# Performance work log

Hardware: AMD Instinct MI355X
Metric: run time of the kernel (lower is better)

The kernel has to match this reference:

```python
import jax, jax.numpy as jnp
import numpy as np

B, S, D, F, E = 4, 2048, 1024, 4096, 4


def setup_inputs() -> dict:
    key = jax.random.key(0)
    ks = jax.random.split(key, 8)
    sd = 1.0 / np.sqrt(D)  # torch Linear default init bound (fan_in = d_model)
    sf = 1.0 / np.sqrt(F)  # fan_in = d_ff
    return {
        "x": jax.random.normal(ks[0], (B, S, D), dtype=jnp.float32),
        # per-expert MLP params, stacked over expert dim E
        "W1": jax.random.uniform(ks[1], (E, D, F), jnp.float32, -sd, sd),
        "b1": jax.random.uniform(ks[2], (E, F), jnp.float32, -sd, sd),
        "W2": jax.random.uniform(ks[3], (E, F, D), jnp.float32, -sf, sf),
        "b2": jax.random.uniform(ks[4], (E, D), jnp.float32, -sf, sf),
        # uncertainty head: Linear(d_model, 1)
        "Wu": jax.random.uniform(ks[5], (D, 1), jnp.float32, -sd, sd),
        "bu": jax.random.uniform(ks[6], (1,), jnp.float32, -sd, sd),
    }


def reference(x, W1, b1, W2, b2, Wu, bu):
    # x: [B, S, D]
    n_exp = W1.shape[0]
    seq = x.shape[1]

    # uncertainty in (0,1), per token: sigmoid(Linear(x)).squeeze(-1)
    u = jax.nn.sigmoid(jnp.einsum("bsd,do->bso", x, Wu) + bu)[..., 0]  # [B,S]
    # variable number of experts per token in [1, E]
    k = jnp.clip(jnp.ceil(u * n_exp), 1, n_exp).astype(jnp.int32)  # [B,S]

    # dense all-expert MLP: every expert processes every token (faithful math;
    # original gathers only active tokens, but per-token result is identical)
    h = jax.nn.relu(jnp.einsum("bsd,edf->bsef", x, W1) + b1)  # [B,S,E,F]
    y = jnp.einsum("bsef,efd->bsed", h, W2) + b2               # [B,S,E,D]

    s_idx = jnp.arange(seq)
    out = jnp.zeros_like(x)
    for i in range(1, n_exp + 1):  # loop over small fixed expert count
        # expert assigned at pass i depends only on position: (s + i - 1) % E
        e_idx = (s_idx + i - 1) % n_exp  # [S]
        y_i = jnp.take_along_axis(y, e_idx[None, :, None, None], axis=2)[:, :, 0, :]  # [B,S,D]
        w = jnp.where(k >= i, u / i, 0.0)  # [B,S]
        out = out + w[..., None] * y_i
    return out
```

## Files before the change

### kernel.cpp

```cpp
#include <hip/hip_runtime.h>

#define DEV __device__ __forceinline__

typedef __attribute__((ext_vector_type(8))) short s16x8;
typedef __attribute__((ext_vector_type(4))) float f32x4;
typedef __attribute__((ext_vector_type(4))) unsigned short u16x4;

#define BTOK 8192
#define DD   1024
#define FF   4096
#define EE   4
#define BK   64

DEV unsigned short f2bf(float f) {
  unsigned int u = __float_as_uint(f);
  unsigned int r = (u + 0x7FFFu + ((u >> 16) & 1u)) >> 16;
  return (unsigned short)r;
}

DEV void gld_lds16(const void* g, void* l) {
  __builtin_amdgcn_global_load_lds(
      (const __attribute__((address_space(1))) unsigned int*)g,
      (__attribute__((address_space(3))) unsigned int*)l,
      16, 0, 0);
}

DEV void gemm_ring(const unsigned short* __restrict__ A,
                   const unsigned short* __restrict__ B,
                   int K, int tileM, int tileN,
                   unsigned short* Ls,
                   f32x4 (&acc)[8][4]) {
  const int t    = threadIdx.x;
  const int lane = t & 63;
  const int wid  = t >> 6;
  const int wr   = wid >> 2;
  const int wc   = wid & 3;
  const int m16  = lane & 15;
  const int quad = lane >> 4;

  const int rT   = t >> 3;
  const int cSrc = (((t & 7) ^ (rT & 7)) << 3);
  const unsigned short* Ag = A + (size_t)(tileM + rT) * K + cSrc;
  const unsigned short* Bg = B + (size_t)(tileN + rT) * K + cSrc;
  const int dOff = t * 8;

  const int sw0 = (((0 * 64 + quad * 16) ^ ((m16 & 7) << 4)) >> 1);
  const int sw1 = (((1 * 64 + quad * 16) ^ ((m16 & 7) << 4)) >> 1);

  const int NT = K / BK;

#define STAGE(kt_)                                                            \
  {                                                                           \
    const int bq_ = ((kt_) & 1) << 15;                  \
    const size_t ko_ = (size_t)(kt_) * BK;                                    \
    _Pragma("unroll") for (int j = 0; j < 4; ++j) {                           \
      gld_lds16(Ag + (size_t)j * 64 * K + ko_, Ls + bq_ + j * 4096 + dOff);   \
      gld_lds16(Bg + (size_t)j * 64 * K + ko_,                                \
                Ls + bq_ + 16384 + j * 4096 + dOff);                          \
    }                                                                         \
  }

#define LOAD_A(mh_)                                                           \
  {                                                                           \
    _Pragma("unroll") for (int ms = 0; ms < 4; ++ms) {                        \
      const int rb_ = Ab + ((wr * 128 + (mh_)*64 + ms * 16 + m16) << 6);      \
      aF[ms * 2 + 0] = *(const s16x8*)(Ls + rb_ + sw0);                       \
      aF[ms * 2 + 1] = *(const s16x8*)(Ls + rb_ + sw1);                       \
    }                                                                         \
  }

#define LOAD_B(nh_)                                                           \
  {                                                                           \
    _Pragma("unroll") for (int ns = 0; ns < 2; ++ns) {                        \
      const int rb_ = Bb + ((wc * 64 + (nh_)*32 + ns * 16 + m16) << 6);       \
      bF[ns * 2 + 0] = *(const s16x8*)(Ls + rb_ + sw0);                       \
      bF[ns * 2 + 1] = *(const s16x8*)(Ls + rb_ + sw1);                       \
    }                                                                         \
  }

#define MFMA_Q(mh_, nh_)                                                      \
  {                                                                           \
    __builtin_amdgcn_s_setprio(1);                                            \
    _Pragma("unroll") for (int ms = 0; ms < 4; ++ms)                          \
        _Pragma("unroll") for (int ns = 0; ns < 2; ++ns) {                    \
      acc[(mh_)*4 + ms][(nh_)*2 + ns] =                                       \
          __builtin_amdgcn_mfma_f32_16x16x32_bf16(                            \
              aF[ms * 2 + 0], bF[ns * 2 + 0],                                 \
              acc[(mh_)*4 + ms][(nh_)*2 + ns], 0, 0, 0);                      \
      acc[(mh_)*4 + ms][(nh_)*2 + ns] =                                       \
          __builtin_amdgcn_mfma_f32_16x16x32_bf16(                            \
              aF[ms * 2 + 1], bF[ns * 2 + 1],                                 \
              acc[(mh_)*4 + ms][(nh_)*2 + ns], 0, 0, 0);                      \
    }                                                                         \
    __builtin_amdgcn_s_setprio(0);                                            \
  }

#define PHASE_BAR()                                                           \
  __builtin_amdgcn_s_barrier();                                               \
  asm volatile("" ::: "memory");                                              \
  __builtin_amdgcn_sched_barrier(0)

  STAGE(0);

  for (int kt = 0; kt < NT; ++kt) {
    if (kt + 1 < NT) {
      STAGE(kt + 1);
      asm volatile("s_waitcnt vmcnt(8)" ::: "memory");
    } else {
      asm volatile("s_waitcnt vmcnt(0)" ::: "memory");
    }
    PHASE_BAR();

    const int Ab = (kt & 1) << 15;
    const int Bb = Ab + 16384;
    s16x8 aF[8], bF[4];

    LOAD_A(0); LOAD_B(0); MFMA_Q(0, 0);
    PHASE_BAR();
    LOAD_B(1); MFMA_Q(0, 1);
    PHASE_BAR();
    LOAD_A(1); MFMA_Q(1, 1);
    PHASE_BAR();
    LOAD_B(0); MFMA_Q(1, 0);
    PHASE_BAR();
  }
#undef PHASE_BAR
#undef MFMA_Q
#undef LOAD_B
#undef LOAD_A
#undef STAGE
}

__global__ __launch_bounds__(512, 2) void gemm1_kernel(
    const unsigned short* __restrict__ xb,
    const unsigned short* __restrict__ W1T,
    const float* __restrict__ b1,
    const float* __restrict__ c,
    unsigned short* __restrict__ h,
    int eBase) {
  __shared__ __attribute__((aligned(16))) unsigned short Ls[65536];

  const int bid = blockIdx.x;
  const int r   = bid & 7;
  const int pos = bid >> 3;
  const int rm  = r >> 1;
  const int rn  = r & 1;
  const int tileM = (rm * 8 + (pos >> 3)) * 256;
  const int tileN = (rn * 8 + (pos & 7)) * 256;

  const int e = eBase + blockIdx.z;

  f32x4 acc[8][4];
#pragma unroll
  for (int i = 0; i < 8; ++i)
#pragma unroll
    for (int j = 0; j < 4; ++j) acc[i][j] = f32x4{0.f, 0.f, 0.f, 0.f};

  gemm_ring(xb, W1T + (size_t)e * FF * DD, DD, tileM, tileN, Ls, acc);

  const int t = threadIdx.x;
  const int lane = t & 63, wid = t >> 6;
  const int wr = wid >> 2, wc = wid & 3;
  const int m16 = lane & 15, quad = lane >> 4;
  const float* b1e = b1 + e * FF;
  unsigned short* hs = h + (size_t)blockIdx.z * ((size_t)BTOK * FF);

#pragma unroll
  for (int mt = 0; mt < 8; ++mt) {
    const int row = tileM + wr * 128 + mt * 16 + quad * 4;
    const float cv0 = c[(row + 0) * EE + e];
    const float cv1 = c[(row + 1) * EE + e];
    const float cv2 = c[(row + 2) * EE + e];
    const float cv3 = c[(row + 3) * EE + e];
#pragma unroll
    for (int nt = 0; nt < 4; ++nt) {
      const int col = tileN + wc * 64 + nt * 16 + m16;
      const float bb = b1e[col];
      f32x4 v = acc[mt][nt];
      hs[(size_t)(row + 0) * FF + col] = f2bf(fmaxf(v[0] + bb, 0.f) * cv0);
      hs[(size_t)(row + 1) * FF + col] = f2bf(fmaxf(v[1] + bb, 0.f) * cv1);
      hs[(size_t)(row + 2) * FF + col] = f2bf(fmaxf(v[2] + bb, 0.f) * cv2);
      hs[(size_t)(row + 3) * FF + col] = f2bf(fmaxf(v[3] + bb, 0.f) * cv3);
    }
  }
}

__global__ __launch_bounds__(512, 2) void gemm2_kernel(
    const unsigned short* __restrict__ h,
    const unsigned short* __restrict__ W2T,
    float* __restrict__ out,
    int eBase) {
  __shared__ __attribute__((aligned(16))) unsigned short Ls[65536];

  const int bid = blockIdx.x;
  const int r   = bid & 7;
  const int pos = bid >> 3;
  const int tileM = (r * 4 + (pos >> 2)) * 256;
  const int tileN = (pos & 3) * 256;

  const int e = eBase + blockIdx.z;

  f32x4 acc[8][4];
#pragma unroll
  for (int i = 0; i < 8; ++i)
#pragma unroll
    for (int j = 0; j < 4; ++j) acc[i][j] = f32x4{0.f, 0.f, 0.f, 0.f};

  gemm_ring(h + (size_t)blockIdx.z * BTOK * FF,
            W2T + (size_t)e * DD * FF,
            FF, tileM, tileN, Ls, acc);

  const int t = threadIdx.x;
  const int lane = t & 63, wid = t >> 6;
  const int wr = wid >> 2, wc = wid & 3;
  const int m16 = lane & 15, quad = lane >> 4;

#pragma unroll
  for (int mt = 0; mt < 8; ++mt) {
    const int row = tileM + wr * 128 + mt * 16 + quad * 4;
#pragma unroll
    for (int nt = 0; nt < 4; ++nt) {
      const int col = tileN + wc * 64 + nt * 16 + m16;
      f32x4 v = acc[mt][nt];
      atomicAdd(&out[(size_t)(row + 0) * DD + col], v[0]);
      atomicAdd(&out[(size_t)(row + 1) * DD + col], v[1]);
      atomicAdd(&out[(size_t)(row + 2) * DD + col], v[2]);
      atomicAdd(&out[(size_t)(row + 3) * DD + col], v[3]);
    }
  }
}

__global__ __launch_bounds__(256) void u_kernel(
    const float* __restrict__ x,
    const float* __restrict__ Wu,
    const float* __restrict__ bu,
    const float* __restrict__ b2,
    float* __restrict__ c,
    float* __restrict__ out) {
  const int tok = blockIdx.x;
  const int tid = threadIdx.x;
  const float* xr = x + (size_t)tok * DD;

  f32x4 xv = ((const f32x4*)xr)[tid];
  f32x4 wv = ((const f32x4*)Wu)[tid];
  float s = xv[0] * wv[0] + xv[1] * wv[1] + xv[2] * wv[2] + xv[3] * wv[3];
#pragma unroll
  for (int off = 32; off > 0; off >>= 1) s += __shfl_down(s, off);

  __shared__ float red[4];
  __shared__ float cL[4];
  if ((tid & 63) == 0) red[tid >> 6] = s;
  __syncthreads();
  if (tid == 0) {
    float dot = red[0] + red[1] + red[2] + red[3] + bu[0];
    float u = 1.f / (1.f + expf(-dot));
    float kf = ceilf(u * 4.f);
    kf = fminf(fmaxf(kf, 1.f), 4.f);
    int k = (int)kf;
    int s4 = tok & 3;
#pragma unroll
    for (int e = 0; e < EE; ++e) {
      int i = ((e - s4) & 3) + 1;
      float ce = (i <= k) ? (u / (float)i) : 0.f;
      cL[e] = ce;
      c[tok * EE + e] = ce;
    }
  }
  __syncthreads();
  const float c0 = cL[0], c1 = cL[1], c2 = cL[2], c3 = cL[3];
#pragma unroll
  for (int d = tid; d < DD; d += 256)
    out[(size_t)tok * DD + d] =
        c0 * b2[d] + c1 * b2[DD + d] + c2 * b2[2 * DD + d] + c3 * b2[3 * DD + d];
}

__global__ __launch_bounds__(256) void cvt_kernel(const float* __restrict__ in,
                                                  unsigned short* __restrict__ ob,
                                                  int n4) {
  int i = blockIdx.x * 256 + threadIdx.x;
  if (i >= n4) return;
  f32x4 a = ((const f32x4*)in)[i];
  u16x4 o = {f2bf(a[0]), f2bf(a[1]), f2bf(a[2]), f2bf(a[3])};
  ((u16x4*)ob)[i] = o;
}

__global__ __launch_bounds__(256) void tpose_kernel(const float* __restrict__ src,
                                                    unsigned short* __restrict__ dst,
                                                    int R, int C) {
  __shared__ float tile[32][33];
  const int e = blockIdx.z;
  const int r0 = blockIdx.y * 32, c0 = blockIdx.x * 32;
  const int tx = threadIdx.x & 31, ty = threadIdx.x >> 5;
  const float* s = src + (size_t)e * R * C;
  unsigned short* d = dst + (size_t)e * C * R;
#pragma unroll
  for (int j = 0; j < 32; j += 8)
    tile[ty + j][tx] = s[(size_t)(r0 + ty + j) * C + (c0 + tx)];
  __syncthreads();
#pragma unroll
  for (int j = 0; j < 32; j += 8)
    d[(size_t)(c0 + ty + j) * R + (r0 + tx)] = f2bf(tile[tx][ty + j]);
}

extern "C" void kernel_launch(void* const* d_in, const int* in_sizes, int n_in,
                              void* d_out, int out_size, void* d_ws, size_t ws_size,
                              hipStream_t stream) {
  const float* x  = (const float*)d_in[0];
  const float* W1 = (const float*)d_in[1];
  const float* b1 = (const float*)d_in[2];
  const float* W2 = (const float*)d_in[3];
  const float* b2 = (const float*)d_in[4];
  const float* Wu = (const float*)d_in[5];
  const float* bu = (const float*)d_in[6];
  float* out = (float*)d_out;

  char* w = (char*)d_ws;
  unsigned short* xb  = (unsigned short*)w;  w += (size_t)BTOK * DD * 2;
  unsigned short* W1T = (unsigned short*)w;  w += (size_t)EE * DD * FF * 2;
  unsigned short* W2T = (unsigned short*)w;  w += (size_t)EE * FF * DD * 2;
  float* c = (float*)w;                      w += (size_t)BTOK * EE * 4;
  unsigned short* h = (unsigned short*)w;
  size_t used = (size_t)(w - (char*)d_ws);
  size_t hOne = (size_t)BTOK * FF * 2;

  size_t avail = (ws_size > used) ? (ws_size - used) : 0;
  int hSlots = (int)(avail / hOne);
  if (hSlots < 1) hSlots = 1;
  if (hSlots > EE) hSlots = EE;

  cvt_kernel<<<(BTOK * DD / 4 + 255) / 256, 256, 0, stream>>>(x, xb, BTOK * DD / 4);
  tpose_kernel<<<dim3(FF / 32, DD / 32, EE), 256, 0, stream>>>(W1, W1T, DD, FF);
  tpose_kernel<<<dim3(DD / 32, FF / 32, EE), 256, 0, stream>>>(W2, W2T, FF, DD);
  u_kernel<<<BTOK, 256, 0, stream>>>(x, Wu, bu, b2, c, out);

  for (int g = 0; g < EE; g += hSlots) {
    int cnt = (EE - g < hSlots) ? (EE - g) : hSlots;
    gemm1_kernel<<<dim3(512, 1, cnt), 512, 0, stream>>>(xb, W1T, b1, c, h, g);
    gemm2_kernel<<<dim3(128, 1, cnt), 512, 0, stream>>>(h, W2T, out, g);
  }
}
```

Baseline: 868.0 us.

## Interleave next-tile global-to-LDS prefetch across MFMA phases in GEMM core

Restructures the double-buffered GEMM main loop so the next K-tile's global-to-LDS loads are split into small groups and issued between the LDS fragment reads and MFMA phases, instead of all at the top of each iteration. The vmcnt wait moves to the end of the iteration with a single drain, and the sched_barrier fences are removed. The goal is to spread memory issue across compute and give the compiler scheduling freedom. In exchange it waits for all outstanding loads each iteration (vmcnt(0)), so less load latency can stay in flight across iterations.

New measurement: 769.3 us. -11.4%, faster.

```diff
diff --git a/kernel.cpp b/kernel.cpp
--- a/kernel.cpp
+++ b/kernel.cpp
@@ -25,7 +25,7 @@
       16, 0, 0);
 }
 
-DEV void gemm_ring(const unsigned short* __restrict__ A,
+DEV void gemm_core(const unsigned short* __restrict__ A,
                    const unsigned short* __restrict__ B,
                    int K, int tileM, int tileN,
                    unsigned short* Ls,
@@ -44,91 +44,105 @@
   const unsigned short* Bg = B + (size_t)(tileN + rT) * K + cSrc;
   const int dOff = t * 8;
 
-  const int sw0 = (((0 * 64 + quad * 16) ^ ((m16 & 7) << 4)) >> 1);
-  const int sw1 = (((1 * 64 + quad * 16) ^ ((m16 & 7) << 4)) >> 1);
+  const int sw0 = ((( 0 + quad * 16) ^ ((m16 & 7) << 4)) >> 1);
+  const int sw1 = (((64 + quad * 16) ^ ((m16 & 7) << 4)) >> 1);
 
   const int NT = K / BK;
 
-#define STAGE(kt_)                                                            \
-  {                                                                           \
-    const int bq_ = ((kt_) & 1) << 15;                  \
-    const size_t ko_ = (size_t)(kt_) * BK;                                    \
-    _Pragma("unroll") for (int j = 0; j < 4; ++j) {                           \
-      gld_lds16(Ag + (size_t)j * 64 * K + ko_, Ls + bq_ + j * 4096 + dOff);   \
-      gld_lds16(Bg + (size_t)j * 64 * K + ko_,                                \
-                Ls + bq_ + 16384 + j * 4096 + dOff);                          \
-    }                                                                         \
-  }
-
-#define LOAD_A(mh_)                                                           \
+#define BAR()                                                                 \
+  __builtin_amdgcn_s_barrier();                                               \
+  asm volatile("" ::: "memory")
+
+#define LOAD_A(dst_, mh_)                                                     \
   {                                                                           \
     _Pragma("unroll") for (int ms = 0; ms < 4; ++ms) {                        \
       const int rb_ = Ab + ((wr * 128 + (mh_)*64 + ms * 16 + m16) << 6);      \
-      aF[ms * 2 + 0] = *(const s16x8*)(Ls + rb_ + sw0);                       \
-      aF[ms * 2 + 1] = *(const s16x8*)(Ls + rb_ + sw1);                       \
+      dst_[ms * 2 + 0] = *(const s16x8*)(Ls + rb_ + sw0);                     \
+      dst_[ms * 2 + 1] = *(const s16x8*)(Ls + rb_ + sw1);                     \
     }                                                                         \
   }
 
-#define LOAD_B(nh_)                                                           \
+#define LOAD_B(dst_, nh_)                                                     \
   {                                                                           \
     _Pragma("unroll") for (int ns = 0; ns < 2; ++ns) {                        \
       const int rb_ = Bb + ((wc * 64 + (nh_)*32 + ns * 16 + m16) << 6);       \
-      bF[ns * 2 + 0] = *(const s16x8*)(Ls + rb_ + sw0);                       \
-      bF[ns * 2 + 1] = *(const s16x8*)(Ls + rb_ + sw1);                       \
+      dst_[ns * 2 + 0] = *(const s16x8*)(Ls + rb_ + sw0);                     \
+      dst_[ns * 2 + 1] = *(const s16x8*)(Ls + rb_ + sw1);                     \
     }                                                                         \
   }
 
-#define MFMA_Q(mh_, nh_)                                                      \
+#define MFMA_Q(aS_, bS_, mh_, nh_)                                            \
   {                                                                           \
     __builtin_amdgcn_s_setprio(1);                                            \
     _Pragma("unroll") for (int ms = 0; ms < 4; ++ms)                          \
         _Pragma("unroll") for (int ns = 0; ns < 2; ++ns) {                    \
       acc[(mh_)*4 + ms][(nh_)*2 + ns] =                                       \
           __builtin_amdgcn_mfma_f32_16x16x32_bf16(                            \
-              aF[ms * 2 + 0], bF[ns * 2 + 0],                                 \
+              aS_[ms * 2 + 0], bS_[ns * 2 + 0],                               \
               acc[(mh_)*4 + ms][(nh_)*2 + ns], 0, 0, 0);                      \
       acc[(mh_)*4 + ms][(nh_)*2 + ns] =                                       \
           __builtin_amdgcn_mfma_f32_16x16x32_bf16(                            \
-              aF[ms * 2 + 1], bF[ns * 2 + 1],                                 \
+              aS_[ms * 2 + 1], bS_[ns * 2 + 1],                               \
               acc[(mh_)*4 + ms][(nh_)*2 + ns], 0, 0, 0);                      \
     }                                                                         \
     __builtin_amdgcn_s_setprio(0);                                            \
   }
 
-#define PHASE_BAR()                                                           \
-  __builtin_amdgcn_s_barrier();                                               \
-  asm volatile("" ::: "memory");                                              \
-  __builtin_amdgcn_sched_barrier(0)
-
-  STAGE(0);
+#define STG_A(j_)                                                             \
+  gld_lds16(Ag + (size_t)(j_) * 64 * K + koN, Ls + bN + (j_)*4096 + dOff)
+#define STG_B(j_)                                                             \
+  gld_lds16(Bg + (size_t)(j_) * 64 * K + koN, Ls + bN + 16384 + (j_)*4096 + dOff)
+
+  {
+#pragma unroll
+    for (int j = 0; j < 4; ++j) {
+      gld_lds16(Ag + (size_t)j * 64 * K, Ls + j * 4096 + dOff);
+      gld_lds16(Bg + (size_t)j * 64 * K, Ls + 16384 + j * 4096 + dOff);
+    }
+    asm volatile("s_waitcnt vmcnt(0)" ::: "memory");
+    BAR();
+  }
 
   for (int kt = 0; kt < NT; ++kt) {
-    if (kt + 1 < NT) {
-      STAGE(kt + 1);
-      asm volatile("s_waitcnt vmcnt(8)" ::: "memory");
-    } else {
-      asm volatile("s_waitcnt vmcnt(0)" ::: "memory");
-    }
-    PHASE_BAR();
-
     const int Ab = (kt & 1) << 15;
     const int Bb = Ab + 16384;
+    const int bN = ((kt + 1) & 1) << 15;
+    const size_t koN = (size_t)(kt + 1) * BK;
+    const bool pf = (kt + 1 < NT);
+
     s16x8 aF[8], bF[4];
 
-    LOAD_A(0); LOAD_B(0); MFMA_Q(0, 0);
-    PHASE_BAR();
-    LOAD_B(1); MFMA_Q(0, 1);
-    PHASE_BAR();
-    LOAD_A(1); MFMA_Q(1, 1);
-    PHASE_BAR();
-    LOAD_B(0); MFMA_Q(1, 0);
-    PHASE_BAR();
-  }
-#undef PHASE_BAR
+    LOAD_A(aF, 0);
+    LOAD_B(bF, 0);
+    if (pf) { STG_A(0); STG_A(1); STG_A(2); }
+    BAR();
+    MFMA_Q(aF, bF, 0, 0);
+
+    LOAD_B(bF, 1);
+    if (pf) { STG_A(3); STG_B(0); STG_B(1); }
+    BAR();
+    MFMA_Q(aF, bF, 0, 1);
+
+    LOAD_A(aF, 1);
+    if (pf) { STG_B(2); STG_B(3); }
+    BAR();
+    MFMA_Q(aF, bF, 1, 1);
+
+    LOAD_B(bF, 0);
+    BAR();
+    MFMA_Q(aF, bF, 1, 0);
+
+    if (pf) {
+      asm volatile("s_waitcnt vmcnt(0)" ::: "memory");
+      BAR();
+    }
+  }
+#undef STG_B
+#undef STG_A
 #undef MFMA_Q
 #undef LOAD_B
 #undef LOAD_A
-#undef STAGE
+#undef BAR
 }
 
 __global__ __launch_bounds__(512, 2) void gemm1_kernel(
@@ -156,7 +170,7 @@
 #pragma unroll
     for (int j = 0; j < 4; ++j) acc[i][j] = f32x4{0.f, 0.f, 0.f, 0.f};
 
-  gemm_ring(xb, W1T + (size_t)e * FF * DD, DD, tileM, tileN, Ls, acc);
+  gemm_core(xb, W1T + (size_t)e * FF * DD, DD, tileM, tileN, Ls, acc);
 
   const int t = threadIdx.x;
   const int lane = t & 63, wid = t >> 6;
@@ -206,7 +220,7 @@
 #pragma unroll
     for (int j = 0; j < 4; ++j) acc[i][j] = f32x4{0.f, 0.f, 0.f, 0.f};
 
-  gemm_ring(h + (size_t)blockIdx.z * BTOK * FF,
+  gemm_core(h + (size_t)blockIdx.z * BTOK * FF,
             W2T + (size_t)e * DD * FF,
             FF, tileM, tileN, Ls, acc);
 
```
